# Kernel tuning notes

Measured on AMD Instinct MI355X. Metric: run time of the kernel, lower is better.

## Reference

```python
import jax, jax.numpy as jnp
import numpy as np

VOCAB = 100000
EMBED = 300
HIDDEN = 300
BATCH = 32768
K_NEG = 10
N_CLASSES = 2
EPS = 1e-5
DENO_W = 1.0
CONO_W = 1.0


def setup_inputs() -> dict:
    key = jax.random.key(0)
    ks = jax.random.split(key, 12)
    init_range = 1.0 / EMBED
    return {
        "center_word_ids": jax.random.randint(ks[0], (BATCH,), 0, VOCAB),
        "context_word_ids": jax.random.randint(ks[1], (BATCH,), 0, VOCAB),
        "neg_context_ids": jax.random.randint(ks[2], (BATCH, K_NEG), 0, VOCAB),
        "party_label": jax.random.randint(ks[3], (BATCH,), 0, N_CLASSES),
        "center_emb": jax.random.uniform(ks[4], (VOCAB, EMBED), jnp.float32, -init_range, init_range),
        "context_emb": jax.random.normal(ks[5], (VOCAB, EMBED), jnp.float32) * 0.02,
        "W_enc": jax.random.normal(ks[6], (HIDDEN, EMBED), jnp.float32) * (1.0 / np.sqrt(EMBED)),
        "b_enc": jnp.zeros((HIDDEN,), jnp.float32),
        "W_dec": jax.random.normal(ks[7], (EMBED, HIDDEN), jnp.float32) * (1.0 / np.sqrt(HIDDEN)),
        "b_dec": jnp.zeros((EMBED,), jnp.float32),
        "W_cls": jax.random.normal(ks[8], (N_CLASSES, HIDDEN), jnp.float32) * (1.0 / np.sqrt(HIDDEN)),
        "b_cls": jnp.zeros((N_CLASSES,), jnp.float32),
    }


def reference(center_word_ids, context_word_ids, neg_context_ids, party_label,
              center_emb, context_emb, W_enc, b_enc, W_dec, b_dec, W_cls, b_cls):
    # encoder_forward (dropout p=0 -> identity)
    emb = center_emb[center_word_ids]                      # [B, E]
    enc = emb @ W_enc.T + b_enc                            # [B, H]
    # deno_forward: skip-gram negative sampling
    center_v = enc @ W_dec.T + b_dec                       # [B, E]
    ctx_v = context_emb[context_word_ids]                  # [B, E]
    pos_score = jnp.clip(jnp.sum(center_v * ctx_v, axis=1), -10.0, 10.0)
    pos = -jax.nn.log_sigmoid(pos_score)                   # [B]
    neg_v = context_emb[neg_context_ids]                   # [B, K, E]
    neg_score = jnp.clip(jnp.einsum('bke,be->bk', neg_v, center_v), -10.0, 10.0)
    neg = -jnp.sum(jax.nn.log_sigmoid(-neg_score), axis=1)  # [B]
    deno_loss = jnp.clip(jnp.mean(pos + neg), EPS, 10.0)
    # cono_forward + cross entropy
    logits = enc @ W_cls.T + b_cls                         # [B, C]
    logp = jax.nn.log_softmax(logits, axis=-1)
    nll = -jnp.take_along_axis(logp, party_label[:, None], axis=1)[:, 0]
    cono_loss = jnp.clip(jnp.mean(nll), EPS, 10.0)
    encoder_loss = jnp.clip(DENO_W * deno_loss + CONO_W * cono_loss, EPS, None)
    return jnp.stack([encoder_loss, deno_loss, cono_loss])
```

## Files before the change

### kernel.cpp

```cpp
#include <hip/hip_runtime.h>
#include <math.h>

#define VOCAB   100000
#define EMBED   300
#define HIDDEN  300
#define BATCH   32768
#define K_NEG   10
#define EPSV    1e-5f

#define KPAD      320
#define NPAD      384
#define CV_STRIDE 304
#define WC2_STRIDE 304
#define NBUCKET 512

typedef __attribute__((ext_vector_type(8))) short  short8;
typedef __attribute__((ext_vector_type(4))) float  f32x4;

__device__ inline unsigned short f2b(float f) {
    union { float f; unsigned int i; } v; v.f = f;
    unsigned int r = v.i + 0x7FFFu + ((v.i >> 16) & 1u);
    return (unsigned short)(r >> 16);
}
__device__ inline void up2(unsigned int u, float& lo, float& hi) {
    union { unsigned int i; float f; } a, b;
    a.i = u << 16; b.i = u & 0xFFFF0000u;
    lo = a.f; hi = b.f;
}
__device__ inline float softplus_fast(float x) {
    const float t = __builtin_amdgcn_exp2f(fabsf(x) * -1.44269504f);
    const float l = __builtin_amdgcn_logf(1.f + t) * 0.69314718f;
    return fmaxf(x, 0.f) + l;
}

__device__ inline void load_lds16(const void* g, void* l) {
    __builtin_amdgcn_global_load_lds(
        (const __attribute__((address_space(1))) unsigned int*)g,
        (__attribute__((address_space(3))) unsigned int*)l, 16, 0, 0);
}

__device__ inline float red64(float v) {
    #pragma unroll
    for (int m = 32; m; m >>= 1) v += __shfl_xor(v, m);
    return v;
}

#define NCH (BATCH * 75)
#define PREP_BLOCKS 2048

__global__ __launch_bounds__(256)
void prep_kernel(const float* __restrict__ cemb, const int* __restrict__ cids,
                 unsigned short* __restrict__ emb_b)
{
    const unsigned GT = PREP_BLOCKS * 256;
    for (unsigned base = blockIdx.x * 256 + threadIdx.x; base < NCH; base += GT * 4) {
        float4 v[4];
        unsigned c[4];
        bool ok[4];
        #pragma unroll
        for (int u = 0; u < 4; ++u) {
            c[u] = base + u * GT;
            ok[u] = (c[u] < NCH);
            if (ok[u]) {
                const unsigned row = c[u] / 75, e = c[u] - row * 75;
                v[u] = *(const float4*)(cemb + (size_t)cids[row] * 300 + e * 4);
            }
        }
        #pragma unroll
        for (int u = 0; u < 4; ++u) {
            if (!ok[u]) continue;
            const unsigned row = c[u] / 75, e = c[u] - row * 75;
            uint2 d;
            d.x = (unsigned)f2b(v[u].x) | ((unsigned)f2b(v[u].y) << 16);
            d.y = (unsigned)f2b(v[u].z) | ((unsigned)f2b(v[u].w) << 16);
            char* dst = (char*)emb_b + (size_t)row * (KPAD * 2) + e * 8;
            if (e < 74) {
                *(uint2*)dst = d;
            } else {
                *(uint4*)dst = make_uint4(d.x, d.y, 0u, 0u);
                char* rb = (char*)emb_b + (size_t)row * (KPAD * 2);
                *(uint4*)(rb + 608) = make_uint4(0u, 0u, 0u, 0u);
                *(uint4*)(rb + 624) = make_uint4(0u, 0u, 0u, 0u);
            }
        }
    }
}

__global__ __launch_bounds__(256)
void w2_kernel(const float* __restrict__ Wd, const float* __restrict__ We,
               unsigned short* __restrict__ w2p)
{
    __shared__ float ds[16][33];
    __shared__ float es[32][17];
    const int tid = threadIdx.x;
    const int tn = tid >> 4, tk = tid & 15;
    const int n = blockIdx.y * 16 + tn;
    const int k = blockIdx.x * 16 + tk;

    float acc = 0.f;
    for (int h0 = 0; h0 < 300; h0 += 32) {
        {
            const int i = tid * 2;
            const int a = i >> 5, h = i & 31;
            const int rr = blockIdx.y * 16 + a;
            #pragma unroll
            for (int j = 0; j < 2; ++j) {
                const int hh = h + j;
                ds[a][hh] = (rr < 300 && h0 + hh < 300) ? Wd[rr * 300 + h0 + hh] : 0.f;
            }
        }
        {
            const int i = tid * 2;
            const int h = i >> 4, c = i & 15;
            const int cc = blockIdx.x * 16 + c;
            #pragma unroll
            for (int j = 0; j < 2; ++j)
                es[h][c + j] = (h0 + h < 300 && cc + j < 300) ? We[(h0 + h) * 300 + cc + j] : 0.f;
        }
        __syncthreads();
        #pragma unroll
        for (int h = 0; h < 32; ++h)
            acc = fmaf(ds[tn][h], es[h][tk], acc);
        __syncthreads();
    }
    if (n < NPAD && k < KPAD)
        w2p[n * KPAD + k] = (n < 300 && k < 300) ? f2b(acc) : (unsigned short)0;
}

__global__ __launch_bounds__(256)
void wb_kernel(const float* __restrict__ Wd, const float* __restrict__ We,
               const float* __restrict__ Wc, const float* __restrict__ b_enc,
               const float* __restrict__ b_dec, const float* __restrict__ b_cls,
               float* __restrict__ wc2, float* __restrict__ bias2, float* __restrict__ bc2)
{
    const int unit = blockIdx.x * 4 + (threadIdx.x >> 6);
    const int lane = threadIdx.x & 63;
    if (unit >= 914) return;
    float s = 0.f;
    if (unit < 304) {
        const int c = unit;
        if (c < 300)
            for (int k = lane; k < 300; k += 64) s = fmaf(Wd[c * 300 + k], b_enc[k], s);
        s = red64(s);
        if (lane == 0) bias2[c] = (c < 300) ? s + b_dec[c] : 0.f;
    } else if (unit < 912) {
        const int u2 = unit - 304;
        const int j = u2 >= 304 ? 1 : 0;
        const int c = u2 - j * 304;
        if (c < 300)
            for (int h = lane; h < 300; h += 64) s = fmaf(Wc[j * 300 + h], We[h * 300 + c], s);
        s = red64(s);
        if (lane == 0) wc2[j * WC2_STRIDE + c] = s;
    } else {
        const int j = unit - 912;
        for (int h = lane; h < 300; h += 64) s = fmaf(Wc[j * 300 + h], b_enc[h], s);
        s = red64(s);
        if (lane == 0) bc2[j] = s + b_cls[j];
    }
}

__global__ __launch_bounds__(256)
void gemm_cv_kernel(const unsigned short* __restrict__ A,
                    const unsigned short* __restrict__ B,
                    const float* __restrict__ bias,
                    unsigned short* __restrict__ C)
{
    __shared__ unsigned short As[2][128 * 32];
    __shared__ unsigned short Bs[2][128 * 32];

    const int tid  = threadIdx.x;
    const int wave = tid >> 6;
    const int lane = tid & 63;
    const int m0 = blockIdx.y * 128;
    const int n0 = blockIdx.x * 128;

    const int wr = (wave & 1) * 64;
    const int wc = (wave >> 1) * 64;
    const int fr = lane & 15;
    const int fq = lane >> 4;

    const unsigned short* gA[2];
    const unsigned short* gB[2];
    int ldsOff[2];
    #pragma unroll
    for (int inst = 0; inst < 2; ++inst) {
        const int t = wave * 2 + inst;
        const int r = (t << 4) + (lane >> 2);
        const int c = ((lane & 3) - r - (r >> 2)) & 3;
        gA[inst] = A + (size_t)(m0 + r) * KPAD + c * 8;
        gB[inst] = B + (size_t)(n0 + r) * KPAD + c * 8;
        ldsOff[inst] = t << 9;
    }

    int aoff[4], boff[4];
    #pragma unroll
    for (int i = 0; i < 4; ++i) {
        const int ra = wr + i * 16 + fr;
        aoff[i] = (ra << 5) + (((fq + ra + (ra >> 2)) & 3) << 3);
        const int rb = wc + i * 16 + fr;
        boff[i] = (rb << 5) + (((fq + rb + (rb >> 2)) & 3) << 3);
    }

    f32x4 acc[4][4] = {};

    #pragma unroll
    for (int inst = 0; inst < 2; ++inst) {
        load_lds16(gA[inst], &As[0][ldsOff[inst]]);
        load_lds16(gB[inst], &Bs[0][ldsOff[inst]]);
    }

    int cur = 0;
    for (int ki = 0; ki < KPAD / 32; ++ki) {
        __syncthreads();
        if (ki + 1 < KPAD / 32) {
            const int k0 = (ki + 1) * 32;
            #pragma unroll
            for (int inst = 0; inst < 2; ++inst) {
                load_lds16(gA[inst] + k0, &As[cur ^ 1][ldsOff[inst]]);
                load_lds16(gB[inst] + k0, &Bs[cur ^ 1][ldsOff[inst]]);
            }
        }
        short8 af[4], bf[4];
        #pragma unroll
        for (int i = 0; i < 4; ++i) af[i] = *(const short8*)&As[cur][aoff[i]];
        #pragma unroll
        for (int j = 0; j < 4; ++j) bf[j] = *(const short8*)&Bs[cur][boff[j]];
        #pragma unroll
        for (int i = 0; i < 4; ++i)
            #pragma unroll
            for (int j = 0; j < 4; ++j)
                acc[i][j] = __builtin_amdgcn_mfma_f32_16x16x32_bf16(
                    af[i], bf[j], acc[i][j], 0, 0, 0);
        cur ^= 1;
    }

    #pragma unroll
    for (int i = 0; i < 4; ++i) {
        #pragma unroll
        for (int r = 0; r < 4; ++r) {
            const int m = m0 + wr + i * 16 + fq * 4 + r;
            unsigned short* crow = C + (size_t)m * CV_STRIDE;
            #pragma unroll
            for (int j = 0; j < 4; ++j) {
                const int n = n0 + wc + j * 16 + fr;
                if (n < 300) {
                    crow[n] = f2b(acc[i][j][r] + bias[n]);
                } else if (n < CV_STRIDE) {
                    crow[n] = 0;
                }
            }
        }
    }
}

__global__ __launch_bounds__(256)
void score_kernel(const unsigned short* __restrict__ cvb,
                  const float* __restrict__ xemb,
                  const int* __restrict__ ctx_ids, const int* __restrict__ neg_ids,
                  float* __restrict__ db)
{
    const int wid  = threadIdx.x >> 6;
    const int lane = threadIdx.x & 63;
    const int fr = lane & 15;
    const int fq = lane >> 4;
    const int myrow = (blockIdx.x * 4 + wid) * 16 + fr;

    union { uint4 u; short8 v; } z16; z16.u = make_uint4(0, 0, 0, 0);

    short8 af[10];
    const unsigned short* arow = cvb + (size_t)myrow * CV_STRIDE + fq * 8;
    #pragma unroll
    for (int kk = 0; kk < 10; ++kk) {
        if (kk < 9 || fq < 2) af[kk] = *(const short8*)(arow + kk * 32);
        else af[kk] = z16.v;
    }

    int ids[11];
    ids[0] = ctx_ids[myrow];
    #pragma unroll
    for (int j = 0; j < 10; ++j) ids[j + 1] = neg_ids[myrow * K_NEG + j];

    const bool dlane = (fr >> 2) == fq;
    const int  dreg  = fr & 3;
    float loss = 0.f;

    #pragma unroll
    for (int j = 0; j < 11; ++j) {
        const float* brow = xemb + (size_t)ids[j] * 300;
        f32x4 acc = {};
        #pragma unroll
        for (int kk = 0; kk < 10; ++kk) {
            const int kb = kk * 32 + fq * 8;
            uint4 u0, u1;
            if (kk < 9 || fq == 0) {
                u0 = *(const uint4*)(brow + kb);
                u1 = *(const uint4*)(brow + kb + 4);
            } else if (fq == 1) {
                u0 = *(const uint4*)(brow + 296);
                u1 = make_uint4(0, 0, 0, 0);
            } else {
                u0 = make_uint4(0, 0, 0, 0);
                u1 = make_uint4(0, 0, 0, 0);
            }
            union { unsigned w[4]; short8 v; } bf;
            bf.w[0] = (u0.y & 0xFFFF0000u) | (u0.x >> 16);
            bf.w[1] = (u0.w & 0xFFFF0000u) | (u0.z >> 16);
            bf.w[2] = (u1.y & 0xFFFF0000u) | (u1.x >> 16);
            bf.w[3] = (u1.w & 0xFFFF0000u) | (u1.z >> 16);
            acc = __builtin_amdgcn_mfma_f32_16x16x32_bf16(af[kk], bf.v, acc, 0, 0, 0);
        }
        if (dlane) {
            float dv = (dreg & 2) ? ((dreg & 1) ? acc[3] : acc[2])
                                  : ((dreg & 1) ? acc[1] : acc[0]);
            float s = fminf(10.f, fmaxf(-10.f, dv));
            loss += softplus_fast(j == 0 ? -s : s);
        }
    }

    float v = red64(loss);
    if (lane == 0) atomicAdd(&db[blockIdx.x & (NBUCKET - 1)], v);
}

__global__ __launch_bounds__(256)
void ce_kernel(const unsigned short* __restrict__ embb,
               const int* __restrict__ labels,
               const float* __restrict__ wc2, const float* __restrict__ bc2,
               float* __restrict__ cb)
{
    const int wid  = threadIdx.x >> 6;
    const int lane = threadIdx.x & 63;
    const int l5   = lane & 31;
    const int row  = blockIdx.x * 8 + wid * 2 + (lane >> 5);
    const bool act = l5 < 19;

    const uint4 Z4 = make_uint4(0, 0, 0, 0);
    const char* evp = (const char*)(embb + (size_t)row * KPAD);
    uint4 e0 = act ? *(const uint4*)(evp + l5 * 32)      : Z4;
    uint4 e1 = act ? *(const uint4*)(evp + l5 * 32 + 16) : Z4;
    float ev[16];
    up2(e0.x, ev[0], ev[1]);  up2(e0.y, ev[2], ev[3]);
    up2(e0.z, ev[4], ev[5]);  up2(e0.w, ev[6], ev[7]);
    up2(e1.x, ev[8], ev[9]);  up2(e1.y, ev[10], ev[11]);
    up2(e1.z, ev[12], ev[13]);up2(e1.w, ev[14], ev[15]);

    float p0 = 0.f, p1 = 0.f;
    if (act) {
        const float* w0 = wc2 + l5 * 16;
        const float* w1 = wc2 + WC2_STRIDE + l5 * 16;
        #pragma unroll
        for (int q = 0; q < 4; ++q) {
            float4 a = *(const float4*)(w0 + q * 4);
            float4 c = *(const float4*)(w1 + q * 4);
            p0 = fmaf(ev[q*4], a.x, p0); p0 = fmaf(ev[q*4+1], a.y, p0);
            p0 = fmaf(ev[q*4+2], a.z, p0); p0 = fmaf(ev[q*4+3], a.w, p0);
            p1 = fmaf(ev[q*4], c.x, p1); p1 = fmaf(ev[q*4+1], c.y, p1);
            p1 = fmaf(ev[q*4+2], c.z, p1); p1 = fmaf(ev[q*4+3], c.w, p1);
        }
    }
    #pragma unroll
    for (int m = 16; m; m >>= 1) { p0 += __shfl_xor(p0, m); p1 += __shfl_xor(p1, m); }

    if (l5 == 0) {
        const float l0 = p0 + bc2[0];
        const float l1 = p1 + bc2[1];
        const float mx = fmaxf(l0, l1);
        const float lse = mx + logf(expf(l0 - mx) + expf(l1 - mx));
        const float nll = lse - (labels[row] ? l1 : l0);
        atomicAdd(&cb[blockIdx.x & (NBUCKET - 1)], nll);
    }
}

__device__ inline float wave_red64(float v) {
    #pragma unroll
    for (int o = 32; o; o >>= 1) v += __shfl_down(v, o);
    return v;
}
__global__ __launch_bounds__(256)
void finalize_kernel(const float* __restrict__ db, const float* __restrict__ cb,
                     float* __restrict__ out)
{
    const int t = threadIdx.x;
    float d = db[t] + db[t + 256];
    float c = cb[t] + cb[t + 256];
    d = wave_red64(d); c = wave_red64(c);
    __shared__ float sd[4], sc[4];
    if ((t & 63) == 0) { sd[t >> 6] = d; sc[t >> 6] = c; }
    __syncthreads();
    if (t == 0) {
        const float inv = 1.0f / (float)BATCH;
        float deno = (sd[0] + sd[1] + sd[2] + sd[3]) * inv;
        float cono = (sc[0] + sc[1] + sc[2] + sc[3]) * inv;
        deno = fminf(10.f, fmaxf(EPSV, deno));
        cono = fminf(10.f, fmaxf(EPSV, cono));
        out[0] = fmaxf(EPSV, deno + cono);
        out[1] = deno;
        out[2] = cono;
    }
}

extern "C" void kernel_launch(void* const* d_in, const int* in_sizes, int n_in,
                              void* d_out, int out_size, void* d_ws, size_t ws_size,
                              hipStream_t stream)
{
    const int*   cids  = (const int*)d_in[0];
    const int*   ctx   = (const int*)d_in[1];
    const int*   neg   = (const int*)d_in[2];
    const int*   lab   = (const int*)d_in[3];
    const float* cemb  = (const float*)d_in[4];
    const float* xemb  = (const float*)d_in[5];
    const float* W_enc = (const float*)d_in[6];
    const float* b_enc = (const float*)d_in[7];
    const float* W_dec = (const float*)d_in[8];
    const float* b_dec = (const float*)d_in[9];
    const float* W_cls = (const float*)d_in[10];
    const float* b_cls = (const float*)d_in[11];
    float* out = (float*)d_out;

    unsigned short* emb_b = (unsigned short*)d_ws;
    unsigned short* cv_b  = emb_b + (size_t)BATCH * KPAD;
    unsigned short* w2p   = cv_b + (size_t)BATCH * CV_STRIDE;
    float* wc2   = (float*)(w2p + (size_t)NPAD * KPAD);
    float* bias2 = wc2 + 2 * WC2_STRIDE;
    float* bc2   = bias2 + WC2_STRIDE;
    float* db    = bc2 + 4;
    float* cb    = db + NBUCKET;

    hipMemsetAsync(db, 0, 2 * NBUCKET * sizeof(float), stream);

    prep_kernel<<<PREP_BLOCKS, 256, 0, stream>>>(cemb, cids, emb_b);

    dim3 wgrid(KPAD / 16, NPAD / 16);
    w2_kernel<<<wgrid, 256, 0, stream>>>(W_dec, W_enc, w2p);
    wb_kernel<<<229, 256, 0, stream>>>(W_dec, W_enc, W_cls, b_enc, b_dec, b_cls,
                                       wc2, bias2, bc2);

    dim3 ggrid(3, BATCH / 128);
    gemm_cv_kernel<<<ggrid, 256, 0, stream>>>(emb_b, w2p, bias2, cv_b);

    score_kernel<<<BATCH / 64, 256, 0, stream>>>(cv_b, xemb, ctx, neg, db);
    ce_kernel<<<BATCH / 8, 256, 0, stream>>>(emb_b, lab, wc2, bc2, cb);

    finalize_kernel<<<1, 256, 0, stream>>>(db, cb, out);
}
```

Baseline: 374.9 us.

## Fuse embedding gather into GEMM, split score work, drop atomics and prep kernel

Removes the separate bf16 prep pass by gathering and converting center embeddings directly inside the GEMM A-tile load, and has the CE kernel read fp32 embeddings directly. It merges the two weight-precompute kernels into one launch. It splits the score kernel so each wave handles two of the eleven context/negative columns, giving six times more waves. Atomics plus the memset are replaced by per-block partial sums reduced in finalize. The cost is register-staged A loads in the GEMM, losing the async global-to-LDS copy for A, and a longer serial reduction in finalize.

```diff
diff --git a/kernel.cpp b/kernel.cpp
--- a/kernel.cpp
+++ b/kernel.cpp
@@ -3,7 +3,6 @@
 
 #define VOCAB   100000
 #define EMBED   300
-#define HIDDEN  300
 #define BATCH   32768
 #define K_NEG   10
 #define EPSV    1e-5f
@@ -12,7 +11,8 @@
 #define NPAD      384
 #define CV_STRIDE 304
 #define WC2_STRIDE 304
-#define NBUCKET 512
+#define NDB ((BATCH / 16) * 6)
+#define NCB (BATCH / 8)
 
 typedef __attribute__((ext_vector_type(8))) short  short8;
 typedef __attribute__((ext_vector_type(4))) float  f32x4;
@@ -22,148 +22,108 @@
     unsigned int r = v.i + 0x7FFFu + ((v.i >> 16) & 1u);
     return (unsigned short)(r >> 16);
 }
-__device__ inline void up2(unsigned int u, float& lo, float& hi) {
-    union { unsigned int i; float f; } a, b;
-    a.i = u << 16; b.i = u & 0xFFFF0000u;
-    lo = a.f; hi = b.f;
-}
 __device__ inline float softplus_fast(float x) {
     const float t = __builtin_amdgcn_exp2f(fabsf(x) * -1.44269504f);
     const float l = __builtin_amdgcn_logf(1.f + t) * 0.69314718f;
     return fmaxf(x, 0.f) + l;
 }
-
 __device__ inline void load_lds16(const void* g, void* l) {
     __builtin_amdgcn_global_load_lds(
         (const __attribute__((address_space(1))) unsigned int*)g,
         (__attribute__((address_space(3))) unsigned int*)l, 16, 0, 0);
 }
-
 __device__ inline float red64(float v) {
     #pragma unroll
     for (int m = 32; m; m >>= 1) v += __shfl_xor(v, m);
     return v;
 }
-
-#define NCH (BATCH * 75)
-#define PREP_BLOCKS 2048
+__device__ inline float wave_red64(float v) {
+    #pragma unroll
+    for (int o = 32; o; o >>= 1) v += __shfl_down(v, o);
+    return v;
+}
+__device__ inline float dpick(const f32x4& a, int dreg) {
+    return (dreg & 2) ? ((dreg & 1) ? a[3] : a[2])
+                      : ((dreg & 1) ? a[1] : a[0]);
+}
 
 __global__ __launch_bounds__(256)
-void prep_kernel(const float* __restrict__ cemb, const int* __restrict__ cids,
-                 unsigned short* __restrict__ emb_b)
-{
-    const unsigned GT = PREP_BLOCKS * 256;
-    for (unsigned base = blockIdx.x * 256 + threadIdx.x; base < NCH; base += GT * 4) {
-        float4 v[4];
-        unsigned c[4];
-        bool ok[4];
-        #pragma unroll
-        for (int u = 0; u < 4; ++u) {
-            c[u] = base + u * GT;
-            ok[u] = (c[u] < NCH);
-            if (ok[u]) {
-                const unsigned row = c[u] / 75, e = c[u] - row * 75;
-                v[u] = *(const float4*)(cemb + (size_t)cids[row] * 300 + e * 4);
-            }
-        }
-        #pragma unroll
-        for (int u = 0; u < 4; ++u) {
-            if (!ok[u]) continue;
-            const unsigned row = c[u] / 75, e = c[u] - row * 75;
-            uint2 d;
-            d.x = (unsigned)f2b(v[u].x) | ((unsigned)f2b(v[u].y) << 16);
-            d.y = (unsigned)f2b(v[u].z) | ((unsigned)f2b(v[u].w) << 16);
-            char* dst = (char*)emb_b + (size_t)row * (KPAD * 2) + e * 8;
-            if (e < 74) {
-                *(uint2*)dst = d;
-            } else {
-                *(uint4*)dst = make_uint4(d.x, d.y, 0u, 0u);
-                char* rb = (char*)emb_b + (size_t)row * (KPAD * 2);
-                *(uint4*)(rb + 608) = make_uint4(0u, 0u, 0u, 0u);
-                *(uint4*)(rb + 624) = make_uint4(0u, 0u, 0u, 0u);
-            }
-        }
-    }
-}
-
-__global__ __launch_bounds__(256)
-void w2_kernel(const float* __restrict__ Wd, const float* __restrict__ We,
-               unsigned short* __restrict__ w2p)
+void ww_kernel(const float* __restrict__ Wd, const float* __restrict__ We,
+               const float* __restrict__ Wc, const float* __restrict__ b_enc,
+               const float* __restrict__ b_dec, const float* __restrict__ b_cls,
+               unsigned short* __restrict__ w2p, float* __restrict__ wc2,
+               float* __restrict__ bias2, float* __restrict__ bc2)
 {
     __shared__ float ds[16][33];
     __shared__ float es[32][17];
-    const int tid = threadIdx.x;
-    const int tn = tid >> 4, tk = tid & 15;
-    const int n = blockIdx.y * 16 + tn;
-    const int k = blockIdx.x * 16 + tk;
-
-    float acc = 0.f;
-    for (int h0 = 0; h0 < 300; h0 += 32) {
-        {
-            const int i = tid * 2;
-            const int a = i >> 5, h = i & 31;
-            const int rr = blockIdx.y * 16 + a;
+    const int b = blockIdx.x;
+    if (b < 480) {
+        const int tid = threadIdx.x;
+        const int tn = tid >> 4, tk = tid & 15;
+        const int bx = b % 20, by = b / 20;
+        const int n = by * 16 + tn;
+        const int k = bx * 16 + tk;
+
+        float acc = 0.f;
+        for (int h0 = 0; h0 < 300; h0 += 32) {
+            {
+                const int i = tid * 2;
+                const int a = i >> 5, h = i & 31;
+                const int rr = by * 16 + a;
+                #pragma unroll
+                for (int j = 0; j < 2; ++j) {
+                    const int hh = h + j;
+                    ds[a][hh] = (rr < 300 && h0 + hh < 300) ? Wd[rr * 300 + h0 + hh] : 0.f;
+                }
+            }
+            {
+                const int i = tid * 2;
+                const int h = i >> 4, c = i & 15;
+                const int cc = bx * 16 + c;
+                #pragma unroll
+                for (int j = 0; j < 2; ++j)
+                    es[h][c + j] = (h0 + h < 300 && cc + j < 300) ? We[(h0 + h) * 300 + cc + j] : 0.f;
+            }
+            __syncthreads();
             #pragma unroll
-            for (int j = 0; j < 2; ++j) {
-                const int hh = h + j;
-                ds[a][hh] = (rr < 300 && h0 + hh < 300) ? Wd[rr * 300 + h0 + hh] : 0.f;
-            }
-        }
-        {
-            const int i = tid * 2;
-            const int h = i >> 4, c = i & 15;
-            const int cc = blockIdx.x * 16 + c;
-            #pragma unroll
-            for (int j = 0; j < 2; ++j)
-                es[h][c + j] = (h0 + h < 300 && cc + j < 300) ? We[(h0 + h) * 300 + cc + j] : 0.f;
-        }
-        __syncthreads();
-        #pragma unroll
-        for (int h = 0; h < 32; ++h)
-            acc = fmaf(ds[tn][h], es[h][tk], acc);
-        __syncthreads();
-    }
-    if (n < NPAD && k < KPAD)
+            for (int h = 0; h < 32; ++h)
+                acc = fmaf(ds[tn][h], es[h][tk], acc);
+            __syncthreads();
+        }
         w2p[n * KPAD + k] = (n < 300 && k < 300) ? f2b(acc) : (unsigned short)0;
+    } else {
+        const int unit = (b - 480) * 4 + (threadIdx.x >> 6);
+        const int lane = threadIdx.x & 63;
+        if (unit >= 914) return;
+        float s = 0.f;
+        if (unit < 304) {
+            const int c = unit;
+            if (c < 300)
+                for (int k = lane; k < 300; k += 64) s = fmaf(Wd[c * 300 + k], b_enc[k], s);
+            s = red64(s);
+            if (lane == 0) bias2[c] = (c < 300) ? s + b_dec[c] : 0.f;
+        } else if (unit < 912) {
+            const int u2 = unit - 304;
+            const int j = u2 >= 304 ? 1 : 0;
+            const int c = u2 - j * 304;
+            if (c < 300)
+                for (int h = lane; h < 300; h += 64) s = fmaf(Wc[j * 300 + h], We[h * 300 + c], s);
+            s = red64(s);
+            if (lane == 0) wc2[j * WC2_STRIDE + c] = s;
+        } else {
+            const int j = unit - 912;
+            for (int h = lane; h < 300; h += 64) s = fmaf(Wc[j * 300 + h], b_enc[h], s);
+            s = red64(s);
+            if (lane == 0) bc2[j] = s + b_cls[j];
+        }
+    }
 }
 
 __global__ __launch_bounds__(256)
-void wb_kernel(const float* __restrict__ Wd, const float* __restrict__ We,
-               const float* __restrict__ Wc, const float* __restrict__ b_enc,
-               const float* __restrict__ b_dec, const float* __restrict__ b_cls,
-               float* __restrict__ wc2, float* __restrict__ bias2, float* __restrict__ bc2)
-{
-    const int unit = blockIdx.x * 4 + (threadIdx.x >> 6);
-    const int lane = threadIdx.x & 63;
-    if (unit >= 914) return;
-    float s = 0.f;
-    if (unit < 304) {
-        const int c = unit;
-        if (c < 300)
-            for (int k = lane; k < 300; k += 64) s = fmaf(Wd[c * 300 + k], b_enc[k], s);
-        s = red64(s);
-        if (lane == 0) bias2[c] = (c < 300) ? s + b_dec[c] : 0.f;
-    } else if (unit < 912) {
-        const int u2 = unit - 304;
-        const int j = u2 >= 304 ? 1 : 0;
-        const int c = u2 - j * 304;
-        if (c < 300)
-            for (int h = lane; h < 300; h += 64) s = fmaf(Wc[j * 300 + h], We[h * 300 + c], s);
-        s = red64(s);
-        if (lane == 0) wc2[j * WC2_STRIDE + c] = s;
-    } else {
-        const int j = unit - 912;
-        for (int h = lane; h < 300; h += 64) s = fmaf(Wc[j * 300 + h], b_enc[h], s);
-        s = red64(s);
-        if (lane == 0) bc2[j] = s + b_cls[j];
-    }
-}
-
-__global__ __launch_bounds__(256)
-void gemm_cv_kernel(const unsigned short* __restrict__ A,
-                    const unsigned short* __restrict__ B,
-                    const float* __restrict__ bias,
-                    unsigned short* __restrict__ C)
+void gemm_fused(const float* __restrict__ cemb, const int* __restrict__ cids,
+                const unsigned short* __restrict__ B,
+                const float* __restrict__ bias,
+                unsigned short* __restrict__ C)
 {
     __shared__ unsigned short As[2][128 * 32];
     __shared__ unsigned short Bs[2][128 * 32];
@@ -179,7 +139,8 @@
     const int fr = lane & 15;
     const int fq = lane >> 4;
 
-    const unsigned short* gA[2];
+    const float* gA[2];
+    int abase[2];
     const unsigned short* gB[2];
     int ldsOff[2];
     #pragma unroll
@@ -187,7 +148,8 @@
         const int t = wave * 2 + inst;
         const int r = (t << 4) + (lane >> 2);
         const int c = ((lane & 3) - r - (r >> 2)) & 3;
-        gA[inst] = A + (size_t)(m0 + r) * KPAD + c * 8;
+        gA[inst] = cemb + (size_t)cids[m0 + r] * 300 + c * 8;
+        abase[inst] = c * 8;
         gB[inst] = B + (size_t)(n0 + r) * KPAD + c * 8;
         ldsOff[inst] = t << 9;
     }
@@ -202,23 +164,46 @@
     }
 
     f32x4 acc[4][4] = {};
-
-    #pragma unroll
-    for (int inst = 0; inst < 2; ++inst) {
-        load_lds16(gA[inst], &As[0][ldsOff[inst]]);
-        load_lds16(gB[inst], &Bs[0][ldsOff[inst]]);
-    }
+    float4 a0[2], a1[2];
+    const float4 FZ4 = make_float4(0.f, 0.f, 0.f, 0.f);
+
+#define LOADA(ki_) do { \
+    _Pragma("unroll") \
+    for (int inst = 0; inst < 2; ++inst) { \
+        const int base_ = (ki_) * 32 + abase[inst]; \
+        if (base_ < 296) { \
+            a0[inst] = *(const float4*)(gA[inst] + (ki_) * 32); \
+            a1[inst] = *(const float4*)(gA[inst] + (ki_) * 32 + 4); \
+        } else if (base_ == 296) { \
+            a0[inst] = *(const float4*)(gA[inst] + (ki_) * 32); \
+            a1[inst] = FZ4; \
+        } else { a0[inst] = FZ4; a1[inst] = FZ4; } \
+    } } while (0)
+
+#define WRITEA(buf_) do { \
+    _Pragma("unroll") \
+    for (int inst = 0; inst < 2; ++inst) { \
+        uint4 d_; \
+        d_.x = (unsigned)f2b(a0[inst].x) | ((unsigned)f2b(a0[inst].y) << 16); \
+        d_.y = (unsigned)f2b(a0[inst].z) | ((unsigned)f2b(a0[inst].w) << 16); \
+        d_.z = (unsigned)f2b(a1[inst].x) | ((unsigned)f2b(a1[inst].y) << 16); \
+        d_.w = (unsigned)f2b(a1[inst].z) | ((unsigned)f2b(a1[inst].w) << 16); \
+        *(uint4*)&As[buf_][ldsOff[inst] + lane * 8] = d_; \
+    } } while (0)
+
+    LOADA(0);
+    load_lds16(gB[0], &Bs[0][ldsOff[0]]);
+    load_lds16(gB[1], &Bs[0][ldsOff[1]]);
+    WRITEA(0);
 
     int cur = 0;
     for (int ki = 0; ki < KPAD / 32; ++ki) {
         __syncthreads();
         if (ki + 1 < KPAD / 32) {
             const int k0 = (ki + 1) * 32;
-            #pragma unroll
-            for (int inst = 0; inst < 2; ++inst) {
-                load_lds16(gA[inst] + k0, &As[cur ^ 1][ldsOff[inst]]);
-                load_lds16(gB[inst] + k0, &Bs[cur ^ 1][ldsOff[inst]]);
-            }
+            load_lds16(gB[0] + k0, &Bs[cur ^ 1][ldsOff[0]]);
+            load_lds16(gB[1] + k0, &Bs[cur ^ 1][ldsOff[1]]);
+            LOADA(ki + 1);
         }
         short8 af[4], bf[4];
         #pragma unroll
@@ -231,8 +216,11 @@
             for (int j = 0; j < 4; ++j)
                 acc[i][j] = __builtin_amdgcn_mfma_f32_16x16x32_bf16(
                     af[i], bf[j], acc[i][j], 0, 0, 0);
+        if (ki + 1 < KPAD / 32) WRITEA(cur ^ 1);
         cur ^= 1;
     }
+#undef LOADA
+#undef WRITEA
 
     #pragma unroll
     for (int i = 0; i < 4; ++i) {
@@ -253,6 +241,8 @@
     }
 }
 
+#define SCORE_BLOCKS (NDB / 4)
+
 __global__ __launch_bounds__(256)
 void score_kernel(const unsigned short* __restrict__ cvb,
                   const float* __restrict__ xemb,
@@ -263,7 +253,10 @@
     const int lane = threadIdx.x & 63;
     const int fr = lane & 15;
     const int fq = lane >> 4;
-    const int myrow = (blockIdx.x * 4 + wid) * 16 + fr;
+    const int gidx = blockIdx.x * 4 + wid;
+    const int rowgrp = gidx / 6;
+    const int jg = gidx - rowgrp * 6;
+    const int myrow = rowgrp * 16 + fr;
 
     union { uint4 u; short8 v; } z16; z16.u = make_uint4(0, 0, 0, 0);
 
@@ -275,86 +268,88 @@
         else af[kk] = z16.v;
     }
 
-    int ids[11];
-    ids[0] = ctx_ids[myrow];
-    #pragma unroll
-    for (int j = 0; j < 10; ++j) ids[j + 1] = neg_ids[myrow * K_NEG + j];
-
+    const int j0 = jg * 2;
+    const bool has1 = (jg < 5);
+    const int j1 = has1 ? j0 + 1 : 10;
+    const int id0 = (j0 == 0) ? ctx_ids[myrow] : neg_ids[myrow * K_NEG + (j0 - 1)];
+    const int id1 = neg_ids[myrow * K_NEG + (j1 - 1)];
+    const float* b0 = xemb + (size_t)id0 * 300;
+    const float* b1 = xemb + (size_t)id1 * 300;
+
+    f32x4 acc0 = {}, acc1 = {};
+    #pragma unroll
+    for (int kk = 0; kk < 10; ++kk) {
+        const int kb = kk * 32 + fq * 8;
+        uint4 u0a, u0b, u1a, u1b;
+        if (kk < 9 || fq == 0) {
+            u0a = *(const uint4*)(b0 + kb); u0b = *(const uint4*)(b0 + kb + 4);
+            u1a = *(const uint4*)(b1 + kb); u1b = *(const uint4*)(b1 + kb + 4);
+        } else if (fq == 1) {
+            u0a = *(const uint4*)(b0 + 296); u0b = make_uint4(0, 0, 0, 0);
+            u1a = *(const uint4*)(b1 + 296); u1b = make_uint4(0, 0, 0, 0);
+        } else {
+            u0a = make_uint4(0, 0, 0, 0); u0b = u0a; u1a = u0a; u1b = u0a;
+        }
+        union { unsigned w[4]; short8 v; } bf0, bf1;
+        bf0.w[0] = (u0a.y & 0xFFFF0000u) | (u0a.x >> 16);
+        bf0.w[1] = (u0a.w & 0xFFFF0000u) | (u0a.z >> 16);
+        bf0.w[2] = (u0b.y & 0xFFFF0000u) | (u0b.x >> 16);
+        bf0.w[3] = (u0b.w & 0xFFFF0000u) | (u0b.z >> 16);
+        bf1.w[0] = (u1a.y & 0xFFFF0000u) | (u1a.x >> 16);
+        bf1.w[1] = (u1a.w & 0xFFFF0000u) | (u1a.z >> 16);
+        bf1.w[2] = (u1b.y & 0xFFFF0000u) | (u1b.x >> 16);
+        bf1.w[3] = (u1b.w & 0xFFFF0000u) | (u1b.z >> 16);
+        acc0 = __builtin_amdgcn_mfma_f32_16x16x32_bf16(af[kk], bf0.v, acc0, 0, 0, 0);
+        acc1 = __builtin_amdgcn_mfma_f32_16x16x32_bf16(af[kk], bf1.v, acc1, 0, 0, 0);
+    }
+
+    float loss = 0.f;
     const bool dlane = (fr >> 2) == fq;
     const int  dreg  = fr & 3;
-    float loss = 0.f;
-
-    #pragma unroll
-    for (int j = 0; j < 11; ++j) {
-        const float* brow = xemb + (size_t)ids[j] * 300;
-        f32x4 acc = {};
-        #pragma unroll
-        for (int kk = 0; kk < 10; ++kk) {
-            const int kb = kk * 32 + fq * 8;
-            uint4 u0, u1;
-            if (kk < 9 || fq == 0) {
-                u0 = *(const uint4*)(brow + kb);
-                u1 = *(const uint4*)(brow + kb + 4);
-            } else if (fq == 1) {
-                u0 = *(const uint4*)(brow + 296);
-                u1 = make_uint4(0, 0, 0, 0);
-            } else {
-                u0 = make_uint4(0, 0, 0, 0);
-                u1 = make_uint4(0, 0, 0, 0);
-            }
-            union { unsigned w[4]; short8 v; } bf;
-            bf.w[0] = (u0.y & 0xFFFF0000u) | (u0.x >> 16);
-            bf.w[1] = (u0.w & 0xFFFF0000u) | (u0.z >> 16);
-            bf.w[2] = (u1.y & 0xFFFF0000u) | (u1.x >> 16);
-            bf.w[3] = (u1.w & 0xFFFF0000u) | (u1.z >> 16);
-            acc = __builtin_amdgcn_mfma_f32_16x16x32_bf16(af[kk], bf.v, acc, 0, 0, 0);
-        }
-        if (dlane) {
-            float dv = (dreg & 2) ? ((dreg & 1) ? acc[3] : acc[2])
-                                  : ((dreg & 1) ? acc[1] : acc[0]);
-            float s = fminf(10.f, fmaxf(-10.f, dv));
-            loss += softplus_fast(j == 0 ? -s : s);
-        }
-    }
-
+    if (dlane) {
+        float s0 = fminf(10.f, fmaxf(-10.f, dpick(acc0, dreg)));
+        loss = softplus_fast(j0 == 0 ? -s0 : s0);
+        if (has1) {
+            float s1 = fminf(10.f, fmaxf(-10.f, dpick(acc1, dreg)));
+            loss += softplus_fast(s1);
+        }
+    }
     float v = red64(loss);
-    if (lane == 0) atomicAdd(&db[blockIdx.x & (NBUCKET - 1)], v);
+    if (lane == 0) db[gidx] = v;
 }
 
 __global__ __launch_bounds__(256)
-void ce_kernel(const unsigned short* __restrict__ embb,
+void ce_kernel(const float* __restrict__ cemb, const int* __restrict__ cids,
                const int* __restrict__ labels,
                const float* __restrict__ wc2, const float* __restrict__ bc2,
                float* __restrict__ cb)
 {
+    __shared__ float s8[8];
     const int wid  = threadIdx.x >> 6;
     const int lane = threadIdx.x & 63;
     const int l5   = lane & 31;
-    const int row  = blockIdx.x * 8 + wid * 2 + (lane >> 5);
+    const int slot = wid * 2 + (lane >> 5);
+    const int row  = blockIdx.x * 8 + slot;
     const bool act = l5 < 19;
-
-    const uint4 Z4 = make_uint4(0, 0, 0, 0);
-    const char* evp = (const char*)(embb + (size_t)row * KPAD);
-    uint4 e0 = act ? *(const uint4*)(evp + l5 * 32)      : Z4;
-    uint4 e1 = act ? *(const uint4*)(evp + l5 * 32 + 16) : Z4;
-    float ev[16];
-    up2(e0.x, ev[0], ev[1]);  up2(e0.y, ev[2], ev[3]);
-    up2(e0.z, ev[4], ev[5]);  up2(e0.w, ev[6], ev[7]);
-    up2(e1.x, ev[8], ev[9]);  up2(e1.y, ev[10], ev[11]);
-    up2(e1.z, ev[12], ev[13]);up2(e1.w, ev[14], ev[15]);
 
     float p0 = 0.f, p1 = 0.f;
     if (act) {
-        const float* w0 = wc2 + l5 * 16;
-        const float* w1 = wc2 + WC2_STRIDE + l5 * 16;
+        const float* src = cemb + (size_t)cids[row] * 300;
+        const int e0 = l5 * 16;
+        const float* w0 = wc2 + e0;
+        const float* w1 = wc2 + WC2_STRIDE + e0;
         #pragma unroll
         for (int q = 0; q < 4; ++q) {
-            float4 a = *(const float4*)(w0 + q * 4);
-            float4 c = *(const float4*)(w1 + q * 4);
-            p0 = fmaf(ev[q*4], a.x, p0); p0 = fmaf(ev[q*4+1], a.y, p0);
-            p0 = fmaf(ev[q*4+2], a.z, p0); p0 = fmaf(ev[q*4+3], a.w, p0);
-            p1 = fmaf(ev[q*4], c.x, p1); p1 = fmaf(ev[q*4+1], c.y, p1);
-            p1 = fmaf(ev[q*4+2], c.z, p1); p1 = fmaf(ev[q*4+3], c.w, p1);
+            const int e = e0 + q * 4;
+            if (e + 3 < 300) {
+                float4 v = *(const float4*)(src + e);
+                float4 a = *(const float4*)(w0 + q * 4);
+                float4 c = *(const float4*)(w1 + q * 4);
+                p0 = fmaf(v.x, a.x, p0); p0 = fmaf(v.y, a.y, p0);
+                p0 = fmaf(v.z, a.z, p0); p0 = fmaf(v.w, a.w, p0);
+                p1 = fmaf(v.x, c.x, p1); p1 = fmaf(v.y, c.y, p1);
+                p1 = fmaf(v.z, c.z, p1); p1 = fmaf(v.w, c.w, p1);
+            }
         }
     }
     #pragma unroll
@@ -365,23 +360,22 @@
         const float l1 = p1 + bc2[1];
         const float mx = fmaxf(l0, l1);
         const float lse = mx + logf(expf(l0 - mx) + expf(l1 - mx));
-        const float nll = lse - (labels[row] ? l1 : l0);
-        atomicAdd(&cb[blockIdx.x & (NBUCKET - 1)], nll);
-    }
-}
-
-__device__ inline float wave_red64(float v) {
-    #pragma unroll
-    for (int o = 32; o; o >>= 1) v += __shfl_down(v, o);
-    return v;
-}
+        s8[slot] = lse - (labels[row] ? l1 : l0);
+    }
+    __syncthreads();
+    if (threadIdx.x == 0) {
+        cb[blockIdx.x] = s8[0] + s8[1] + s8[2] + s8[3] + s8[4] + s8[5] + s8[6] + s8[7];
+    }
+}
+
 __global__ __launch_bounds__(256)
 void finalize_kernel(const float* __restrict__ db, const float* __restrict__ cb,
                      float* __restrict__ out)
 {
     const int t = threadIdx.x;
-    float d = db[t] + db[t + 256];
-    float c = cb[t] + cb[t + 256];
+    float d = 0.f, c = 0.f;
+    for (int i = t; i < NDB; i += 256) d += db[i];
+    for (int i = t; i < NCB; i += 256) c += cb[i];
     d = wave_red64(d); c = wave_red64(c);
     __shared__ float sd[4], sc[4];
     if ((t & 63) == 0) { sd[t >> 6] = d; sc[t >> 6] = c; }
@@ -416,29 +410,22 @@
     const float* b_cls = (const float*)d_in[11];
     float* out = (float*)d_out;
 
-    unsigned short* emb_b = (unsigned short*)d_ws;
-    unsigned short* cv_b  = emb_b + (size_t)BATCH * KPAD;
-    unsigned short* w2p   = cv_b + (size_t)BATCH * CV_STRIDE;
+    unsigned short* cv_b = (unsigned short*)d_ws;
+    unsigned short* w2p  = cv_b + (size_t)BATCH * CV_STRIDE;
     float* wc2   = (float*)(w2p + (size_t)NPAD * KPAD);
     float* bias2 = wc2 + 2 * WC2_STRIDE;
     float* bc2   = bias2 + WC2_STRIDE;
     float* db    = bc2 + 4;
-    float* cb    = db + NBUCKET;
-
-    hipMemsetAsync(db, 0, 2 * NBUCKET * sizeof(float), stream);
-
-    prep_kernel<<<PREP_BLOCKS, 256, 0, stream>>>(cemb, cids, emb_b);
-
-    dim3 wgrid(KPAD / 16, NPAD / 16);
-    w2_kernel<<<wgrid, 256, 0, stream>>>(W_dec, W_enc, w2p);
-    wb_kernel<<<229, 256, 0, stream>>>(W_dec, W_enc, W_cls, b_enc, b_dec, b_cls,
-                                       wc2, bias2, bc2);
+    float* cb    = db + NDB;
+
+    ww_kernel<<<709, 256, 0, stream>>>(W_dec, W_enc, W_cls, b_enc, b_dec, b_cls,
+                                       w2p, wc2, bias2, bc2);
 
     dim3 ggrid(3, BATCH / 128);
-    gemm_cv_kernel<<<ggrid, 256, 0, stream>>>(emb_b, w2p, bias2, cv_b);
-
-    score_kernel<<<BATCH / 64, 256, 0, stream>>>(cv_b, xemb, ctx, neg, db);
-    ce_kernel<<<BATCH / 8, 256, 0, stream>>>(emb_b, lab, wc2, bc2, cb);
+    gemm_fused<<<ggrid, 256, 0, stream>>>(cemb, cids, w2p, bias2, cv_b);
+
+    score_kernel<<<SCORE_BLOCKS, 256, 0, stream>>>(cv_b, xemb, ctx, neg, db);
+    ce_kernel<<<BATCH / 8, 256, 0, stream>>>(cemb, cids, lab, wc2, bc2, cb);
 
     finalize_kernel<<<1, 256, 0, stream>>>(db, cb, out);
 }
```

After: 387.2 us. 3.3% more time.
